# Kernel optimization log

Hardware: AMD Instinct MI355X
Metric: run time of the kernel (lower is better)

The kernel has to match this reference:

```python
import jax, jax.numpy as jnp
import numpy as np

B, EMB, P, K = 8192, 768, 96, 256
D = EMB // P  # dsub = 8


def setup_inputs() -> dict:
    key = jax.random.key(0)
    k1, k2 = jax.random.split(key)
    vecs = jax.random.normal(k1, (B, EMB), dtype=jnp.float32)
    # torch init: uniform(-1, 1)
    codebook = jax.random.uniform(k2, (P, K, D), dtype=jnp.float32, minval=-1.0, maxval=1.0)
    return {"vecs": vecs, "codebook": codebook}


def reference(vecs, codebook):
    b = vecs.shape[0]
    p, k, d = codebook.shape
    v = vecs.reshape(b, p, d)                                  # [B,P,D]
    # squared distances via expanded quadratic (avoids [B,P,K,D] broadcast):
    # ||v-c||^2 = ||v||^2 - 2 v.c + ||c||^2
    dots = jnp.einsum('bpd,pkd->bpk', v, codebook)             # [B,P,K]
    d2 = (jnp.sum(v * v, axis=-1, keepdims=True)               # [B,P,1]
          - 2.0 * dots
          + jnp.sum(codebook * codebook, axis=-1)[None])       # [1,P,K]
    proba = jax.nn.softmax(-d2, axis=-1)                       # [B,P,K]
    # straight-through hard assignment
    idx = jnp.argmax(proba, axis=-1)                           # [B,P]
    hard = jax.nn.one_hot(idx, k, dtype=proba.dtype)           # [B,P,K]
    ste = jax.lax.stop_gradient(hard - proba) + proba
    # reconstruct from codebook
    out = jnp.einsum('bpk,pkd->bpd', ste, codebook).reshape(b, p * d)
    return out
```

## Files before the change

kernel.cpp:

```cpp
#include <hip/hip_runtime.h>


#define TPB 256
#define KBQ 4

namespace {
constexpr int kB   = 8192;
constexpr int kEMB = 768;
constexpr int kP   = 96;
constexpr int kK   = 256;
constexpr int kD   = 8;
}

__global__ __launch_bounds__(TPB, 3)
void pq_argmin_kernel(const float* __restrict__ vecs,
                      const float* __restrict__ codebook,
                      float* __restrict__ out)
{
    __shared__ alignas(16) float lds_code[kK][kD];
    __shared__ alignas(16) float lds_c2[kK];

    const int p = blockIdx.y;
    const int t = threadIdx.x;

    {
        const float4* cb4 =
            reinterpret_cast<const float4*>(codebook + (size_t)p * kK * kD);
        float4 a = cb4[2 * t];
        float4 b = cb4[2 * t + 1];
        float c2 = a.x * a.x + a.y * a.y + a.z * a.z + a.w * a.w +
                   b.x * b.x + b.y * b.y + b.z * b.z + b.w * b.w;
        float4* lc = reinterpret_cast<float4*>(&lds_code[t][0]);
        lc[0] = make_float4(-2.0f * a.x, -2.0f * a.y, -2.0f * a.z, -2.0f * a.w);
        lc[1] = make_float4(-2.0f * b.x, -2.0f * b.y, -2.0f * b.z, -2.0f * b.w);
        lds_c2[t] = c2;
    }
    __syncthreads();

    const int b0 = blockIdx.x * (TPB * KBQ) + t;

    float v[KBQ][kD];
#pragma unroll
    for (int q = 0; q < KBQ; ++q) {
        const float4* vp = reinterpret_cast<const float4*>(
            vecs + (size_t)(b0 + q * TPB) * kEMB + p * kD);
        float4 x = vp[0];
        float4 y = vp[1];
        v[q][0] = x.x; v[q][1] = x.y; v[q][2] = x.z; v[q][3] = x.w;
        v[q][4] = y.x; v[q][5] = y.y; v[q][6] = y.z; v[q][7] = y.w;
    }

    float best[KBQ];
    int   bidx[KBQ];
#pragma unroll
    for (int q = 0; q < KBQ; ++q) {
        best[q] = __builtin_inff();
        bidx[q] = 0;
    }

#pragma unroll 4
    for (int k = 0; k < kK; ++k) {
        const float4 c0  = *reinterpret_cast<const float4*>(&lds_code[k][0]);
        const float4 c1  = *reinterpret_cast<const float4*>(&lds_code[k][4]);
        const float  c2k = lds_c2[k];
#pragma unroll
        for (int q = 0; q < KBQ; ++q) {
            float s = fmaf(c0.x, v[q][0], c2k);
            s = fmaf(c0.y, v[q][1], s);
            s = fmaf(c0.z, v[q][2], s);
            s = fmaf(c0.w, v[q][3], s);
            s = fmaf(c1.x, v[q][4], s);
            s = fmaf(c1.y, v[q][5], s);
            s = fmaf(c1.z, v[q][6], s);
            s = fmaf(c1.w, v[q][7], s);
            if (s < best[q]) {
                best[q] = s;
                bidx[q] = k;
            }
        }
    }

#pragma unroll
    for (int q = 0; q < KBQ; ++q) {
        const float4* cr = reinterpret_cast<const float4*>(
            codebook + ((size_t)p * kK + bidx[q]) * kD);
        float4 r0 = cr[0];
        float4 r1 = cr[1];
        float4* op = reinterpret_cast<float4*>(
            out + (size_t)(b0 + q * TPB) * kEMB + p * kD);
        op[0] = r0;
        op[1] = r1;
    }
}

extern "C" void kernel_launch(void* const* d_in, const int* in_sizes, int n_in,
                              void* d_out, int out_size, void* d_ws, size_t ws_size,
                              hipStream_t stream)
{
    const float* vecs     = (const float*)d_in[0];
    const float* codebook = (const float*)d_in[1];
    float* out            = (float*)d_out;

    dim3 grid(kB / (TPB * KBQ), kP, 1);
    dim3 block(TPB, 1, 1);
    hipLaunchKernelGGL(pq_argmin_kernel, grid, block, 0, stream,
                       vecs, codebook, out);
}
```

Before: 123.9 us.

## Use packed FMA scoring with chunked min tracking and LDS-based reconstruction

Computes distance scores with v_pk_fma_f32 on float pairs, moving the -2 scale onto the input vector so the shared codebook holds raw values. The argmin loop now tracks only the best chunk of four codes using fminf, then rescans that chunk at the end to recover the exact index. The output row is read from LDS instead of global memory. This cuts VALU instruction count and compare/select work per code, at the cost of inline asm and a rescan whose score summation order differs slightly from the reference.

```diff
diff --git a/kernel.cpp b/kernel.cpp
--- a/kernel.cpp
+++ b/kernel.cpp
@@ -1,8 +1,12 @@
 #include <hip/hip_runtime.h>
 
 
+typedef float f32x2 __attribute__((ext_vector_type(2)));
+typedef float f32x4 __attribute__((ext_vector_type(4)));
+
 #define TPB 256
 #define KBQ 4
+#define CHUNK 4
 
 namespace {
 constexpr int kB   = 8192;
@@ -12,81 +16,121 @@
 constexpr int kD   = 8;
 }
 
+__device__ __forceinline__ f32x2 pk_fma(f32x2 a, f32x2 b, f32x2 c) {
+    f32x2 d;
+    asm("v_pk_fma_f32 %0, %1, %2, %3" : "=v"(d) : "v"(a), "v"(b), "v"(c));
+    return d;
+}
+
+__device__ __forceinline__ float code_score(const f32x2* cp, const f32x2* vs,
+                                            f32x2 c2z) {
+    f32x2 a = pk_fma(cp[0], vs[0], c2z);
+    a = pk_fma(cp[1], vs[1], a);
+    a = pk_fma(cp[2], vs[2], a);
+    a = pk_fma(cp[3], vs[3], a);
+    return a.x + a.y;
+}
+
 __global__ __launch_bounds__(TPB, 3)
 void pq_argmin_kernel(const float* __restrict__ vecs,
                       const float* __restrict__ codebook,
                       float* __restrict__ out)
 {
     __shared__ alignas(16) float lds_code[kK][kD];
-    __shared__ alignas(16) float lds_c2[kK];
+    __shared__ alignas(16) f32x2 lds_c2z[kK];
 
     const int p = blockIdx.y;
     const int t = threadIdx.x;
 
     {
-        const float4* cb4 =
-            reinterpret_cast<const float4*>(codebook + (size_t)p * kK * kD);
-        float4 a = cb4[2 * t];
-        float4 b = cb4[2 * t + 1];
+        const f32x4* cb = reinterpret_cast<const f32x4*>(
+            codebook + (size_t)p * kK * kD);
+        f32x4 a = cb[2 * t];
+        f32x4 b = cb[2 * t + 1];
         float c2 = a.x * a.x + a.y * a.y + a.z * a.z + a.w * a.w +
                    b.x * b.x + b.y * b.y + b.z * b.z + b.w * b.w;
-        float4* lc = reinterpret_cast<float4*>(&lds_code[t][0]);
-        lc[0] = make_float4(-2.0f * a.x, -2.0f * a.y, -2.0f * a.z, -2.0f * a.w);
-        lc[1] = make_float4(-2.0f * b.x, -2.0f * b.y, -2.0f * b.z, -2.0f * b.w);
-        lds_c2[t] = c2;
+        f32x4* lc = reinterpret_cast<f32x4*>(&lds_code[t][0]);
+        lc[0] = a;
+        lc[1] = b;
+        lds_c2z[t] = f32x2{c2, 0.0f};
     }
     __syncthreads();
 
     const int b0 = blockIdx.x * (TPB * KBQ) + t;
-
-    float v[KBQ][kD];
+    f32x2 vs[KBQ][4];
 #pragma unroll
     for (int q = 0; q < KBQ; ++q) {
-        const float4* vp = reinterpret_cast<const float4*>(
+        const f32x4* vp = reinterpret_cast<const f32x4*>(
             vecs + (size_t)(b0 + q * TPB) * kEMB + p * kD);
-        float4 x = vp[0];
-        float4 y = vp[1];
-        v[q][0] = x.x; v[q][1] = x.y; v[q][2] = x.z; v[q][3] = x.w;
-        v[q][4] = y.x; v[q][5] = y.y; v[q][6] = y.z; v[q][7] = y.w;
+        f32x4 x = vp[0];
+        f32x4 y = vp[1];
+        vs[q][0] = f32x2{-2.0f * x.x, -2.0f * x.y};
+        vs[q][1] = f32x2{-2.0f * x.z, -2.0f * x.w};
+        vs[q][2] = f32x2{-2.0f * y.x, -2.0f * y.y};
+        vs[q][3] = f32x2{-2.0f * y.z, -2.0f * y.w};
     }
 
     float best[KBQ];
-    int   bidx[KBQ];
+    int   bch[KBQ];
 #pragma unroll
     for (int q = 0; q < KBQ; ++q) {
         best[q] = __builtin_inff();
-        bidx[q] = 0;
+        bch[q] = 0;
     }
 
-#pragma unroll 4
-    for (int k = 0; k < kK; ++k) {
-        const float4 c0  = *reinterpret_cast<const float4*>(&lds_code[k][0]);
-        const float4 c1  = *reinterpret_cast<const float4*>(&lds_code[k][4]);
-        const float  c2k = lds_c2[k];
+#pragma unroll 2
+    for (int ch = 0; ch < kK / CHUNK; ++ch) {
+        f32x2 cp[CHUNK][4];
+        f32x2 c2z[CHUNK];
+        {
+            const f32x2* zz = &lds_c2z[ch * CHUNK];
+#pragma unroll
+            for (int c = 0; c < CHUNK; ++c) {
+                const f32x2* cc = reinterpret_cast<const f32x2*>(
+                    &lds_code[ch * CHUNK + c][0]);
+                cp[c][0] = cc[0]; cp[c][1] = cc[1];
+                cp[c][2] = cc[2]; cp[c][3] = cc[3];
+                c2z[c] = zz[c];
+            }
+        }
 #pragma unroll
         for (int q = 0; q < KBQ; ++q) {
-            float s = fmaf(c0.x, v[q][0], c2k);
-            s = fmaf(c0.y, v[q][1], s);
-            s = fmaf(c0.z, v[q][2], s);
-            s = fmaf(c0.w, v[q][3], s);
-            s = fmaf(c1.x, v[q][4], s);
-            s = fmaf(c1.y, v[q][5], s);
-            s = fmaf(c1.z, v[q][6], s);
-            s = fmaf(c1.w, v[q][7], s);
-            if (s < best[q]) {
-                best[q] = s;
-                bidx[q] = k;
+            float s0 = code_score(cp[0], vs[q], c2z[0]);
+            float s1 = code_score(cp[1], vs[q], c2z[1]);
+            float s2 = code_score(cp[2], vs[q], c2z[2]);
+            float s3 = code_score(cp[3], vs[q], c2z[3]);
+            float m = fminf(fminf(fminf(s0, s1), s2), s3);
+            if (m < best[q]) {
+                best[q] = m;
+                bch[q] = ch;
             }
         }
     }
 
 #pragma unroll
     for (int q = 0; q < KBQ; ++q) {
-        const float4* cr = reinterpret_cast<const float4*>(
-            codebook + ((size_t)p * kK + bidx[q]) * kD);
-        float4 r0 = cr[0];
-        float4 r1 = cr[1];
-        float4* op = reinterpret_cast<float4*>(
+        const int base = bch[q] * CHUNK;
+        float s[CHUNK];
+#pragma unroll
+        for (int c = 0; c < CHUNK; ++c) {
+            f32x2 cp[4];
+            const f32x2* cc = reinterpret_cast<const f32x2*>(
+                &lds_code[base + c][0]);
+            cp[0] = cc[0]; cp[1] = cc[1]; cp[2] = cc[2]; cp[3] = cc[3];
+            s[c] = code_score(cp, vs[q], lds_c2z[base + c]);
+        }
+        int idx = base;
+        bool fnd = (s[0] == best[q]);
+#pragma unroll
+        for (int c = 1; c < CHUNK; ++c) {
+            bool e = (s[c] == best[q]) && !fnd;
+            idx = e ? base + c : idx;
+            fnd = fnd || (s[c] == best[q]);
+        }
+        const f32x4* row = reinterpret_cast<const f32x4*>(&lds_code[idx][0]);
+        f32x4 r0 = row[0];
+        f32x4 r1 = row[1];
+        f32x4* op = reinterpret_cast<f32x4*>(
             out + (size_t)(b0 + q * TPB) * kEMB + p * kD);
         op[0] = r0;
         op[1] = r1;
```

Result: slower. 128.4 us (+3.7%).
